# Kernel optimization log

Measured on AMD Instinct MI355X. Metric: run time of the kernel, lower is better.

The kernel has to match this reference:

```python
import jax, jax.numpy as jnp
import numpy as np

# Module hyperparameters (init_kwargs)
D = 2          # input_dim
OUT = 3        # output_dim
T = 14         # log2 hash table size
L = 16         # number of levels
F = 2          # features per level
N_MIN, N_MAX = 16, 512
B = 1048576    # batch of query points
HIDDEN = 64

_b = np.exp((np.log(N_MAX) - np.log(N_MIN)) / (L - 1))
RES = jnp.asarray(np.floor(N_MIN * _b ** np.arange(L)).astype(np.float32))  # [L]

# voxel corner offsets [D, 2^D] (same construction as torch module)
_border = np.empty((D, 2 ** D), dtype=np.int32)
for _i in range(D):
    _border[_i, :] = np.array(([0] * 2 ** _i + [1] * 2 ** _i) * 2 ** (D - _i - 1), dtype=np.int32)
BORDER = jnp.asarray(_border)

# NVIDIA tiny-cuda-nn primes; uint32 arithmetic is exact for the low T bits
# (low 14 bits of a product/xor only depend on low 32 bits), matching torch's
# int64 multiply-xor followed by mod 2^T.
PRIMES = jnp.array([1, 2654435761, 805459861, 3674653429, 2097192037, 1434869437, 2165219737][:D], dtype=jnp.uint32)


def setup_inputs() -> dict:
    key = jax.random.key(0)
    ks = jax.random.split(key, 8)
    x = jax.random.uniform(ks[0], (B, D), jnp.float32)  # coords in [0,1)
    tables = jax.random.uniform(ks[1], (L, 2 ** T, F), jnp.float32, -1e-4, 1e-4)
    W1 = jax.random.normal(ks[2], (HIDDEN, L * F), jnp.float32) * 0.05
    b1 = jnp.zeros((HIDDEN,), jnp.float32)
    W2 = jax.random.normal(ks[3], (HIDDEN, HIDDEN), jnp.float32) * 0.05
    b2 = jnp.zeros((HIDDEN,), jnp.float32)
    W3 = jax.random.normal(ks[4], (OUT, HIDDEN), jnp.float32) * 0.05
    b3 = jnp.zeros((OUT,), jnp.float32)
    return {"x": x, "tables": tables, "W1": W1, "b1": b1, "W2": W2, "b2": b2, "W3": W3, "b3": b3}


def reference(x, tables, W1, b1, W2, b2, W3, b3):
    n = x.shape[0]
    # scale coords by each level resolution: [B, D, L]
    scaled = x[:, :, None] * RES[None, None, :]
    grid = jnp.floor(scaled).astype(jnp.int32)                     # [B, D, L]
    corners = grid[..., None] + BORDER[None, :, None, :]           # [B, D, L, 2^D]
    # spatial hash: xor of coord * prime per dimension, mod 2^T
    h = jnp.zeros((n, L, 2 ** D), jnp.uint32)
    for i in range(D):
        h = h ^ (corners[:, i].astype(jnp.uint32) * PRIMES[i])
    idx = (h & jnp.uint32(2 ** T - 1)).astype(jnp.int32)           # [B, L, 2^D]
    # per-level embedding gather: [B, L, 2^D, F]
    looked = tables[jnp.arange(L)[None, :, None], idx]
    # (bi/tri)linear interpolation weights: prod over dims -> [B, L, 2^D]
    w = jnp.prod(1.0 - jnp.abs(scaled[..., None] - corners.astype(x.dtype)), axis=1)
    feat = jnp.einsum('blc,blcf->blf', w, looked).reshape(n, L * F)  # [B, L*F]
    # small MLP head
    h1 = jax.nn.relu(feat @ W1.T + b1)
    h2 = jax.nn.relu(h1 @ W2.T + b2)
    return h2 @ W3.T + b3
```

## Files before the change

kernel.cpp:

```cpp
#include <hip/hip_runtime.h>
#include <hip/hip_bf16.h>
#include <math.h>


#define TBL_MASK 16383u
#define PRIME1   2654435761u

typedef __attribute__((ext_vector_type(8))) short short8;
typedef __attribute__((ext_vector_type(4))) float f32x4;
typedef __attribute__((ext_vector_type(4))) unsigned int uint4v;

struct ResArr { float r[16]; };

__device__ __forceinline__ unsigned short bf16rn(float f) {
    __hip_bfloat16 h = __float2bfloat16(f);
    return __builtin_bit_cast(unsigned short, h);
}
__device__ __forceinline__ float bf16tof(unsigned short u) {
    unsigned int x = ((unsigned int)u) << 16;
    return __builtin_bit_cast(float, x);
}

__device__ __forceinline__ void splitW(const float* __restrict__ p,
                                       short8& hi, short8& lo) {
    const float4 w0 = *(const float4*)p;
    const float4 w1 = *(const float4*)(p + 4);
    float v[8] = {w0.x, w0.y, w0.z, w0.w, w1.x, w1.y, w1.z, w1.w};
    #pragma unroll
    for (int e = 0; e < 8; ++e) {
        const unsigned short hb = bf16rn(v[e]);
        const unsigned short lb = bf16rn(v[e] - bf16tof(hb));
        hi[e] = (short)hb;
        lo[e] = (short)lb;
    }
}

__device__ __forceinline__ void splitWm(const float* __restrict__ p, bool valid,
                                        short8& hi, short8& lo) {
    float v[8];
    if (valid) {
        const float4 w0 = *(const float4*)p;
        const float4 w1 = *(const float4*)(p + 4);
        v[0] = w0.x; v[1] = w0.y; v[2] = w0.z; v[3] = w0.w;
        v[4] = w1.x; v[5] = w1.y; v[6] = w1.z; v[7] = w1.w;
    } else {
        #pragma unroll
        for (int e = 0; e < 8; ++e) v[e] = 0.0f;
    }
    #pragma unroll
    for (int e = 0; e < 8; ++e) {
        const unsigned short hb = bf16rn(v[e]);
        const unsigned short lb = bf16rn(v[e] - bf16tof(hb));
        hi[e] = (short)hb;
        lo[e] = (short)lb;
    }
}

__device__ __forceinline__ short8 ldsFrag(const unsigned short* p) {
    return __builtin_bit_cast(short8, *(const uint4v*)p);
}

#define MFMA(a, b, c) __builtin_amdgcn_mfma_f32_16x16x32_bf16((a), (b), (c), 0, 0, 0)

__global__ __launch_bounds__(64) void mh_mfma(
    const float* __restrict__ x,
    const float* __restrict__ tables,
    const float* __restrict__ W1,
    const float* __restrict__ b1,
    const float* __restrict__ W2,
    const float* __restrict__ b2,
    const float* __restrict__ W3,
    const float* __restrict__ b3,
    float* __restrict__ out,
    ResArr res, int n)
{
    __shared__ unsigned short sFH[64 * 40];
    __shared__ unsigned short sFL[64 * 40];
    __shared__ unsigned short sAH[32 * 72];
    __shared__ unsigned short sAL[32 * 72];

    const int L  = threadIdx.x;
    const int ln = L & 15;
    const int q  = L >> 4;
    const long base = (long)blockIdx.x * 64;
    long s = base + L;
    if (s >= (long)n) s = (long)n - 1;

    const float2 xv = reinterpret_cast<const float2*>(x)[s];
    const float2* __restrict__ tbl2 = reinterpret_cast<const float2*>(tables);

    #pragma unroll 4
    for (int l = 0; l < 16; ++l) {
        const float r  = res.r[l];
        const float sx = xv.x * r;
        const float sy = xv.y * r;
        const float gx = floorf(sx);
        const float gy = floorf(sy);
        const unsigned ux = (unsigned)(int)gx;
        const unsigned uy = (unsigned)(int)gy;
        const unsigned hy0 = uy * PRIME1;
        const unsigned hy1 = hy0 + PRIME1;
        const unsigned i00 = ( ux       ^ hy0) & TBL_MASK;
        const unsigned i10 = ((ux + 1u) ^ hy0) & TBL_MASK;
        const unsigned i01 = ( ux       ^ hy1) & TBL_MASK;
        const unsigned i11 = ((ux + 1u) ^ hy1) & TBL_MASK;
        const float2* tl = tbl2 + (l << 14);
        const float2 t00 = tl[i00];
        const float2 t10 = tl[i10];
        const float2 t01 = tl[i01];
        const float2 t11 = tl[i11];
        const float wx0 = 1.0f - fabsf(sx - gx);
        const float wx1 = 1.0f - fabsf(sx - (gx + 1.0f));
        const float wy0 = 1.0f - fabsf(sy - gy);
        const float wy1 = 1.0f - fabsf(sy - (gy + 1.0f));
        const float w00 = wx0 * wy0;
        const float w10 = wx1 * wy0;
        const float w01 = wx0 * wy1;
        const float w11 = wx1 * wy1;
        const float f0 = fmaf(w00, t00.x, fmaf(w10, t10.x, fmaf(w01, t01.x, w11 * t11.x)));
        const float f1 = fmaf(w00, t00.y, fmaf(w10, t10.y, fmaf(w01, t01.y, w11 * t11.y)));
        const unsigned short h0 = bf16rn(f0);
        const unsigned short h1e = bf16rn(f1);
        const unsigned short l0 = bf16rn(f0 - bf16tof(h0));
        const unsigned short l1 = bf16rn(f1 - bf16tof(h1e));
        *(unsigned int*)&sFH[L * 40 + 2 * l] = (unsigned)h0 | ((unsigned)h1e << 16);
        *(unsigned int*)&sFL[L * 40 + 2 * l] = (unsigned)l0 | ((unsigned)l1 << 16);
    }

    float b1v[4], b2v[4];
    #pragma unroll
    for (int nt = 0; nt < 4; ++nt) { b1v[nt] = b1[nt * 16 + ln]; b2v[nt] = b2[nt * 16 + ln]; }
    const float b3v = (ln < 3) ? b3[ln] : 0.0f;

    const f32x4 zero4 = {0.0f, 0.0f, 0.0f, 0.0f};

    for (int mh = 0; mh < 2; ++mh) {
        short8 a1h[2], a1l[2];
        #pragma unroll
        for (int mt = 0; mt < 2; ++mt) {
            const int row = mh * 32 + mt * 16 + ln;
            a1h[mt] = ldsFrag(&sFH[row * 40 + q * 8]);
            a1l[mt] = ldsFrag(&sFL[row * 40 + q * 8]);
        }
        f32x4 acc1[2][4];
        #pragma unroll
        for (int mt = 0; mt < 2; ++mt)
            #pragma unroll
            for (int nt = 0; nt < 4; ++nt) acc1[mt][nt] = zero4;

        #pragma unroll
        for (int nt = 0; nt < 4; ++nt) {
            short8 bh, bl;
            splitW(W1 + (nt * 16 + ln) * 32 + q * 8, bh, bl);
            #pragma unroll
            for (int mt = 0; mt < 2; ++mt) {
                f32x4 a = acc1[mt][nt];
                a = MFMA(a1l[mt], bh, a);
                a = MFMA(a1h[mt], bl, a);
                a = MFMA(a1h[mt], bh, a);
                acc1[mt][nt] = a;
            }
        }
        #pragma unroll
        for (int mt = 0; mt < 2; ++mt)
            #pragma unroll
            for (int nt = 0; nt < 4; ++nt) {
                const int col = nt * 16 + ln;
                #pragma unroll
                for (int r = 0; r < 4; ++r) {
                    float v = fmaxf(acc1[mt][nt][r] + b1v[nt], 0.0f);
                    const unsigned short hb = bf16rn(v);
                    const unsigned short lb = bf16rn(v - bf16tof(hb));
                    const int rl = mt * 16 + q * 4 + r;
                    sAH[rl * 72 + col] = hb;
                    sAL[rl * 72 + col] = lb;
                }
            }

        short8 a2h[2][2], a2l[2][2];
        #pragma unroll
        for (int mt = 0; mt < 2; ++mt)
            #pragma unroll
            for (int ks = 0; ks < 2; ++ks) {
                const int row = mt * 16 + ln;
                a2h[mt][ks] = ldsFrag(&sAH[row * 72 + ks * 32 + q * 8]);
                a2l[mt][ks] = ldsFrag(&sAL[row * 72 + ks * 32 + q * 8]);
            }
        f32x4 acc2[2][4];
        #pragma unroll
        for (int mt = 0; mt < 2; ++mt)
            #pragma unroll
            for (int nt = 0; nt < 4; ++nt) acc2[mt][nt] = zero4;

        #pragma unroll
        for (int nt = 0; nt < 4; ++nt)
            #pragma unroll
            for (int ks = 0; ks < 2; ++ks) {
                short8 bh, bl;
                splitW(W2 + (nt * 16 + ln) * 64 + ks * 32 + q * 8, bh, bl);
                #pragma unroll
                for (int mt = 0; mt < 2; ++mt) {
                    f32x4 a = acc2[mt][nt];
                    a = MFMA(a2l[mt][ks], bh, a);
                    a = MFMA(a2h[mt][ks], bl, a);
                    a = MFMA(a2h[mt][ks], bh, a);
                    acc2[mt][nt] = a;
                }
            }
        #pragma unroll
        for (int mt = 0; mt < 2; ++mt)
            #pragma unroll
            for (int nt = 0; nt < 4; ++nt) {
                const int col = nt * 16 + ln;
                #pragma unroll
                for (int r = 0; r < 4; ++r) {
                    float v = fmaxf(acc2[mt][nt][r] + b2v[nt], 0.0f);
                    const unsigned short hb = bf16rn(v);
                    const unsigned short lb = bf16rn(v - bf16tof(hb));
                    const int rl = mt * 16 + q * 4 + r;
                    sAH[rl * 72 + col] = hb;
                    sAL[rl * 72 + col] = lb;
                }
            }

        short8 a3h[2][2], a3l[2][2];
        #pragma unroll
        for (int mt = 0; mt < 2; ++mt)
            #pragma unroll
            for (int ks = 0; ks < 2; ++ks) {
                const int row = mt * 16 + ln;
                a3h[mt][ks] = ldsFrag(&sAH[row * 72 + ks * 32 + q * 8]);
                a3l[mt][ks] = ldsFrag(&sAL[row * 72 + ks * 32 + q * 8]);
            }
        f32x4 acc3[2] = {zero4, zero4};
        #pragma unroll
        for (int ks = 0; ks < 2; ++ks) {
            short8 bh, bl;
            splitWm(W3 + ln * 64 + ks * 32 + q * 8, ln < 3, bh, bl);
            #pragma unroll
            for (int mt = 0; mt < 2; ++mt) {
                f32x4 a = acc3[mt];
                a = MFMA(a3l[mt][ks], bh, a);
                a = MFMA(a3h[mt][ks], bl, a);
                a = MFMA(a3h[mt][ks], bh, a);
                acc3[mt] = a;
            }
        }
        if (ln < 3) {
            #pragma unroll
            for (int mt = 0; mt < 2; ++mt)
                #pragma unroll
                for (int r = 0; r < 4; ++r) {
                    const long sg = base + mh * 32 + mt * 16 + q * 4 + r;
                    if (sg < (long)n) out[sg * 3 + ln] = acc3[mt][r] + b3v;
                }
        }
    }
}

extern "C" void kernel_launch(void* const* d_in, const int* in_sizes, int n_in,
                              void* d_out, int out_size, void* d_ws, size_t ws_size,
                              hipStream_t stream) {
    const float* x      = (const float*)d_in[0];
    const float* tables = (const float*)d_in[1];
    const float* W1     = (const float*)d_in[2];
    const float* b1v    = (const float*)d_in[3];
    const float* W2     = (const float*)d_in[4];
    const float* b2v    = (const float*)d_in[5];
    const float* W3     = (const float*)d_in[6];
    const float* b3v    = (const float*)d_in[7];
    float* out = (float*)d_out;

    const int n = in_sizes[0] / 2;

    ResArr ra;
    const double bb = exp((log(512.0) - log(16.0)) / 15.0);
    for (int k = 0; k < 16; ++k) ra.r[k] = (float)floor(16.0 * pow(bb, (double)k));

    dim3 grid((n + 63) / 64), block(64);
    hipLaunchKernelGGL(mh_mfma, grid, block, 0, stream,
                       x, tables, W1, b1v, W2, b2v, W3, b3v, out, ra, n);
}
```

Baseline: 238.0 us.

## Pre-split MLP weights into bf16 hi/lo once and alias LDS buffers

Adds a small pre-kernel that converts W1, W2 and W3 into bf16 high and low parts once, storing them in the workspace. The main kernel then loads ready-made fragments instead of every block redoing the split with VALU conversions. The layer-1 feature fragments for both halves are now loaded into registers up front, which lets the feature and activation LDS buffers share one array and shrinks shared memory per block. A launch-bounds occupancy hint is also added. In exchange there is an extra kernel launch and more register pressure from the hoisted fragments.

New measurement: 290.6 us. 1.22x slower.

```diff
diff --git a/kernel.cpp b/kernel.cpp
--- a/kernel.cpp
+++ b/kernel.cpp
@@ -17,67 +17,64 @@
     return __builtin_bit_cast(unsigned short, h);
 }
 __device__ __forceinline__ float bf16tof(unsigned short u) {
-    unsigned int x = ((unsigned int)u) << 16;
-    return __builtin_bit_cast(float, x);
-}
-
-__device__ __forceinline__ void splitW(const float* __restrict__ p,
-                                       short8& hi, short8& lo) {
-    const float4 w0 = *(const float4*)p;
-    const float4 w1 = *(const float4*)(p + 4);
-    float v[8] = {w0.x, w0.y, w0.z, w0.w, w1.x, w1.y, w1.z, w1.w};
-    #pragma unroll
-    for (int e = 0; e < 8; ++e) {
-        const unsigned short hb = bf16rn(v[e]);
-        const unsigned short lb = bf16rn(v[e] - bf16tof(hb));
-        hi[e] = (short)hb;
-        lo[e] = (short)lb;
-    }
-}
-
-__device__ __forceinline__ void splitWm(const float* __restrict__ p, bool valid,
-                                        short8& hi, short8& lo) {
-    float v[8];
-    if (valid) {
-        const float4 w0 = *(const float4*)p;
-        const float4 w1 = *(const float4*)(p + 4);
-        v[0] = w0.x; v[1] = w0.y; v[2] = w0.z; v[3] = w0.w;
-        v[4] = w1.x; v[5] = w1.y; v[6] = w1.z; v[7] = w1.w;
-    } else {
-        #pragma unroll
-        for (int e = 0; e < 8; ++e) v[e] = 0.0f;
-    }
-    #pragma unroll
-    for (int e = 0; e < 8; ++e) {
-        const unsigned short hb = bf16rn(v[e]);
-        const unsigned short lb = bf16rn(v[e] - bf16tof(hb));
-        hi[e] = (short)hb;
-        lo[e] = (short)lb;
-    }
-}
-
-__device__ __forceinline__ short8 ldsFrag(const unsigned short* p) {
+    unsigned int xx = ((unsigned int)u) << 16;
+    return __builtin_bit_cast(float, xx);
+}
+__device__ __forceinline__ short8 ld8(const unsigned short* p) {
     return __builtin_bit_cast(short8, *(const uint4v*)p);
 }
 
 #define MFMA(a, b, c) __builtin_amdgcn_mfma_f32_16x16x32_bf16((a), (b), (c), 0, 0, 0)
 
-__global__ __launch_bounds__(64) void mh_mfma(
+#define W1H_OFF 0
+#define W1L_OFF 2048
+#define W2H_OFF 4096
+#define W2L_OFF 8192
+#define W3H_OFF 12288
+#define W3L_OFF 13312
+#define WS_USHORTS 14336
+
+__global__ __launch_bounds__(256) void split_weights(
+    const float* __restrict__ W1, const float* __restrict__ W2,
+    const float* __restrict__ W3, unsigned short* __restrict__ ws)
+{
+    const int t = blockIdx.x * blockDim.x + threadIdx.x;
+    const int stride = gridDim.x * blockDim.x;
+    for (int i = t; i < 2048; i += stride) {
+        const float v = W1[i];
+        const unsigned short hb = bf16rn(v);
+        ws[W1H_OFF + i] = hb;
+        ws[W1L_OFF + i] = bf16rn(v - bf16tof(hb));
+    }
+    for (int i = t; i < 4096; i += stride) {
+        const float v = W2[i];
+        const unsigned short hb = bf16rn(v);
+        ws[W2H_OFF + i] = hb;
+        ws[W2L_OFF + i] = bf16rn(v - bf16tof(hb));
+    }
+    for (int i = t; i < 1024; i += stride) {
+        const float v = (i < 192) ? W3[i] : 0.0f;
+        const unsigned short hb = bf16rn(v);
+        ws[W3H_OFF + i] = hb;
+        ws[W3L_OFF + i] = bf16rn(v - bf16tof(hb));
+    }
+}
+
+__global__ __launch_bounds__(64, 4) void mh_mfma(
     const float* __restrict__ x,
     const float* __restrict__ tables,
-    const float* __restrict__ W1,
+    const unsigned short* __restrict__ wsw,
     const float* __restrict__ b1,
-    const float* __restrict__ W2,
     const float* __restrict__ b2,
-    const float* __restrict__ W3,
     const float* __restrict__ b3,
     float* __restrict__ out,
     ResArr res, int n)
 {
-    __shared__ unsigned short sFH[64 * 40];
-    __shared__ unsigned short sFL[64 * 40];
-    __shared__ unsigned short sAH[32 * 72];
-    __shared__ unsigned short sAL[32 * 72];
+    __shared__ __align__(16) unsigned short smem[5120];
+    unsigned short* const sFH = smem;
+    unsigned short* const sFL = smem + 2560;
+    unsigned short* const sAH = smem;
+    unsigned short* const sAL = smem + 2304;
 
     const int L  = threadIdx.x;
     const int ln = L & 15;
@@ -127,6 +124,16 @@
         *(unsigned int*)&sFL[L * 40 + 2 * l] = (unsigned)l0 | ((unsigned)l1 << 16);
     }
 
+    short8 a1h[2][2], a1l[2][2];
+    #pragma unroll
+    for (int mh = 0; mh < 2; ++mh)
+        #pragma unroll
+        for (int mt = 0; mt < 2; ++mt) {
+            const int row = mh * 32 + mt * 16 + ln;
+            a1h[mh][mt] = ld8(&sFH[row * 40 + q * 8]);
+            a1l[mh][mt] = ld8(&sFL[row * 40 + q * 8]);
+        }
+
     float b1v[4], b2v[4];
     #pragma unroll
     for (int nt = 0; nt < 4; ++nt) { b1v[nt] = b1[nt * 16 + ln]; b2v[nt] = b2[nt * 16 + ln]; }
@@ -135,13 +142,6 @@
     const f32x4 zero4 = {0.0f, 0.0f, 0.0f, 0.0f};
 
     for (int mh = 0; mh < 2; ++mh) {
-        short8 a1h[2], a1l[2];
-        #pragma unroll
-        for (int mt = 0; mt < 2; ++mt) {
-            const int row = mh * 32 + mt * 16 + ln;
-            a1h[mt] = ldsFrag(&sFH[row * 40 + q * 8]);
-            a1l[mt] = ldsFrag(&sFL[row * 40 + q * 8]);
-        }
         f32x4 acc1[2][4];
         #pragma unroll
         for (int mt = 0; mt < 2; ++mt)
@@ -150,14 +150,14 @@
 
         #pragma unroll
         for (int nt = 0; nt < 4; ++nt) {
-            short8 bh, bl;
-            splitW(W1 + (nt * 16 + ln) * 32 + q * 8, bh, bl);
+            const short8 bh = ld8(&wsw[W1H_OFF + (nt * 16 + ln) * 32 + q * 8]);
+            const short8 bl = ld8(&wsw[W1L_OFF + (nt * 16 + ln) * 32 + q * 8]);
             #pragma unroll
             for (int mt = 0; mt < 2; ++mt) {
                 f32x4 a = acc1[mt][nt];
-                a = MFMA(a1l[mt], bh, a);
-                a = MFMA(a1h[mt], bl, a);
-                a = MFMA(a1h[mt], bh, a);
+                a = MFMA(a1l[mh][mt], bh, a);
+                a = MFMA(a1h[mh][mt], bl, a);
+                a = MFMA(a1h[mh][mt], bh, a);
                 acc1[mt][nt] = a;
             }
         }
@@ -183,8 +183,8 @@
             #pragma unroll
             for (int ks = 0; ks < 2; ++ks) {
                 const int row = mt * 16 + ln;
-                a2h[mt][ks] = ldsFrag(&sAH[row * 72 + ks * 32 + q * 8]);
-                a2l[mt][ks] = ldsFrag(&sAL[row * 72 + ks * 32 + q * 8]);
+                a2h[mt][ks] = ld8(&sAH[row * 72 + ks * 32 + q * 8]);
+                a2l[mt][ks] = ld8(&sAL[row * 72 + ks * 32 + q * 8]);
             }
         f32x4 acc2[2][4];
         #pragma unroll
@@ -196,8 +196,8 @@
         for (int nt = 0; nt < 4; ++nt)
             #pragma unroll
             for (int ks = 0; ks < 2; ++ks) {
-                short8 bh, bl;
-                splitW(W2 + (nt * 16 + ln) * 64 + ks * 32 + q * 8, bh, bl);
+                const short8 bh = ld8(&wsw[W2H_OFF + (nt * 16 + ln) * 64 + ks * 32 + q * 8]);
+                const short8 bl = ld8(&wsw[W2L_OFF + (nt * 16 + ln) * 64 + ks * 32 + q * 8]);
                 #pragma unroll
                 for (int mt = 0; mt < 2; ++mt) {
                     f32x4 a = acc2[mt][nt];
@@ -229,14 +229,14 @@
             #pragma unroll
             for (int ks = 0; ks < 2; ++ks) {
                 const int row = mt * 16 + ln;
-                a3h[mt][ks] = ldsFrag(&sAH[row * 72 + ks * 32 + q * 8]);
-                a3l[mt][ks] = ldsFrag(&sAL[row * 72 + ks * 32 + q * 8]);
+                a3h[mt][ks] = ld8(&sAH[row * 72 + ks * 32 + q * 8]);
+                a3l[mt][ks] = ld8(&sAL[row * 72 + ks * 32 + q * 8]);
             }
         f32x4 acc3[2] = {zero4, zero4};
         #pragma unroll
         for (int ks = 0; ks < 2; ++ks) {
-            short8 bh, bl;
-            splitWm(W3 + ln * 64 + ks * 32 + q * 8, ln < 3, bh, bl);
+            const short8 bh = ld8(&wsw[W3H_OFF + ln * 64 + ks * 32 + q * 8]);
+            const short8 bl = ld8(&wsw[W3L_OFF + ln * 64 + ks * 32 + q * 8]);
             #pragma unroll
             for (int mt = 0; mt < 2; ++mt) {
                 f32x4 a = acc3[mt];
@@ -270,6 +270,7 @@
     const float* W3     = (const float*)d_in[6];
     const float* b3v    = (const float*)d_in[7];
     float* out = (float*)d_out;
+    unsigned short* wsu = (unsigned short*)d_ws;
 
     const int n = in_sizes[0] / 2;
 
@@ -277,7 +278,9 @@
     const double bb = exp((log(512.0) - log(16.0)) / 15.0);
     for (int k = 0; k < 16; ++k) ra.r[k] = (float)floor(16.0 * pow(bb, (double)k));
 
+    hipLaunchKernelGGL(split_weights, dim3(8), dim3(256), 0, stream, W1, W2, W3, wsu);
+
     dim3 grid((n + 63) / 64), block(64);
     hipLaunchKernelGGL(mh_mfma, grid, block, 0, stream,
-                       x, tables, W1, b1v, W2, b2v, W3, b3v, out, ra, n);
-}
+                       x, tables, wsu, b1v, b2v, b3v, out, ra, n);
+}
```
